# Kernel tuning notes

Measured on AMD Instinct MI355X. Metric: run time of the kernel, lower is better.

## Reference

```python
import jax, jax.numpy as jnp
import numpy as np


def setup_inputs() -> dict:
    key = jax.random.key(0)
    ks = jax.random.split(key, 7)
    B, T, H, O = 2048, 2048, 32, 2
    SCALE = 0.1  # keep gates out of deep saturation
    return {
        "x": jax.random.normal(ks[0], (B, T), dtype=jnp.float32),
        "w_ih": jax.random.normal(ks[1], (3 * H, 1), dtype=jnp.float32) * SCALE,
        "w_hh": jax.random.normal(ks[2], (3 * H, H), dtype=jnp.float32) * SCALE,
        "b_ih": jax.random.normal(ks[3], (3 * H,), dtype=jnp.float32) * SCALE,
        "b_hh": jax.random.normal(ks[4], (3 * H,), dtype=jnp.float32) * SCALE,
        "head_w": jax.random.normal(ks[5], (O, H), dtype=jnp.float32) * SCALE,
        "head_b": jax.random.normal(ks[6], (O,), dtype=jnp.float32) * SCALE,
    }


def reference(x, w_ih, w_hh, b_ih, b_hh, head_w, head_b):
    # x: [B, T] scalar time series (torch does x.unsqueeze(-1)).
    B, T = x.shape
    H = w_hh.shape[1]
    # Precompute input contributions to all 3 gates: [B, T, 3H]
    # (input_size == 1, so this is an outer product with w_ih[:, 0]).
    xg = x[:, :, None] * w_ih[:, 0] + b_ih
    xg_t = jnp.swapaxes(xg, 0, 1)  # [T, B, 3H] for scan

    def step(h, xg_step):
        gh = h @ w_hh.T + b_hh  # [B, 3H]
        xr, xz, xn = jnp.split(xg_step, 3, axis=-1)
        hr, hz, hn = jnp.split(gh, 3, axis=-1)
        r = jax.nn.sigmoid(xr + hr)
        z = jax.nn.sigmoid(xz + hz)
        n = jnp.tanh(xn + r * hn)
        h_new = (1.0 - z) * n + z * h
        return h_new, None

    h0 = jnp.zeros((B, H), dtype=x.dtype)
    hT, _ = jax.lax.scan(step, h0, xg_t)
    # head applied to last timestep's output (== final hidden state)
    return hT @ head_w.T + head_b
```

## Files before the change

kernel.cpp:

```cpp
#include <hip/hip_runtime.h>


typedef _Float16 f16x2 __attribute__((ext_vector_type(2)));

__device__ __forceinline__ float fdot2(int a, int b, float c) {
    return __builtin_amdgcn_fdot2(__builtin_bit_cast(f16x2, a),
                                  __builtin_bit_cast(f16x2, b), c, false);
}

__device__ __forceinline__ int pack_pair(float a, float b) {
    f16x2 p;
    p.x = (_Float16)a;
    p.y = (_Float16)b;
    return __builtin_bit_cast(int, p);
}

template<int CTRL>
__device__ __forceinline__ int dppmov(int src) {
    return __builtin_amdgcn_update_dpp(0, src, CTRL, 0xF, 0xF, true);
}

__global__ __launch_bounds__(64, 1)
void gru_scan_kernel(const float* __restrict__ x,
                     const float* __restrict__ w_ih,
                     const float* __restrict__ w_hh,
                     const float* __restrict__ b_ih,
                     const float* __restrict__ b_hh,
                     const float* __restrict__ head_w,
                     const float* __restrict__ head_b,
                     float* __restrict__ out,
                     int T)
{
    const int l  = (int)threadIdx.x;
    const int gg = (l >> 4) & 1;
    const int m  = (l & 15) + ((l >> 5) << 4);
    const int b  = (int)blockIdx.x * 2 + gg;

    __shared__ float hf_s[2][32];
    __shared__ __align__(16) float x_s[2][2][32];

    bool lowfirst;
    {
        auto pr = __builtin_amdgcn_permlane32_swap((unsigned)l, (unsigned)l,
                                                   false, false);
        lowfirst = ((int)pr[0] == (l & 31));
    }

    const float NL2E  = -1.44269504088896f;
    const float P2L2E =  2.88539008177793f;

    constexpr int M[16] = {0,1,2,3,7,6,5,4,15,14,13,12,8,9,10,11};
    const int c0 = l & 15;

    int wR[16], wZ[16], wN[16];
    {
        const float* pR = w_hh + (     m) * 32;
        const float* pZ = w_hh + (32 + m) * 32;
        const float* pN = w_hh + (64 + m) * 32;
#pragma unroll
        for (int q = 0; q < 16; ++q) {
            const int cc  = c0 ^ M[q];
            const int clo = lowfirst ? cc      : cc + 16;
            const int chi = lowfirst ? cc + 16 : cc;
            wR[q] = pack_pair(NL2E  * pR[clo], NL2E  * pR[chi]);
            wZ[q] = pack_pair(NL2E  * pZ[clo], NL2E  * pZ[chi]);
            wN[q] = pack_pair(P2L2E * pN[clo], P2L2E * pN[chi]);
        }
    }
#pragma unroll
    for (int q = 0; q < 16; ++q) {
        asm volatile("" : "+v"(wR[q]), "+v"(wZ[q]), "+v"(wN[q]));
    }

    const float wihr = NL2E  * w_ih[m];
    const float wihz = NL2E  * w_ih[32 + m];
    const float wihn = P2L2E * w_ih[64 + m];
    const float br   = NL2E  * (b_ih[m]      + b_hh[m]);
    const float bz   = NL2E  * (b_ih[32 + m] + b_hh[32 + m]);
    const float bni  = P2L2E * b_ih[64 + m];
    const float bnh  = P2L2E * b_hh[64 + m];

    const float* xrow   = x + (size_t)b * (size_t)T;
    const int    nchunk = T >> 5;

    float h = 0.0f;
    x_s[gg][0][m] = xrow[m];
    float xnext  = (nchunk > 1) ? xrow[32 + m] : 0.0f;
    __builtin_amdgcn_wave_barrier();

    for (int c = 0; c < nchunk; ++c) {
        const int buf = c & 1;
        const float* xs = &x_s[gg][buf][0];
#pragma unroll 4
        for (int s = 0; s < 32; ++s) {
            const float xv  = xs[s];
            const float hm1 = h - 1.0f;

            const unsigned hf = (unsigned)__builtin_bit_cast(unsigned short,
                                                             (_Float16)h);
            auto sw = __builtin_amdgcn_permlane32_swap(hf, hf, false, false);
            const int o0 = (int)sw[0];
            const int o1 = (int)sw[1];
            const int P0  = (o1 << 16) | o0;
            const int P1  = dppmov<0xB1 >(P0);
            const int P2  = dppmov<0x4E >(P0);
            const int P3  = dppmov<0x4E >(P1);
            const int P4  = dppmov<0x141>(P0);
            const int P5  = dppmov<0x141>(P1);
            const int P6  = dppmov<0x141>(P2);
            const int P7  = dppmov<0x141>(P3);
            const int P8  = dppmov<0x140>(P0);
            const int P9  = dppmov<0x140>(P1);
            const int P10 = dppmov<0x140>(P2);
            const int P11 = dppmov<0x140>(P3);
            const int P12 = dppmov<0x140>(P4);
            const int P13 = dppmov<0x140>(P5);
            const int P14 = dppmov<0x140>(P6);
            const int P15 = dppmov<0x140>(P7);

            float rA = fdot2(P0, wR[0], fmaf(xv, wihr, br));
            float zA = fdot2(P0, wZ[0], fmaf(xv, wihz, bz));
            float nA = fdot2(P0, wN[0], bnh);
            float rB = fdot2(P8, wR[8], 0.0f);
            float zB = fdot2(P8, wZ[8], 0.0f);
            float nB = fdot2(P8, wN[8], 0.0f);
            rA = fdot2(P1, wR[1], rA); zA = fdot2(P1, wZ[1], zA); nA = fdot2(P1, wN[1], nA);
            rB = fdot2(P9, wR[9], rB); zB = fdot2(P9, wZ[9], zB); nB = fdot2(P9, wN[9], nB);
            rA = fdot2(P2, wR[2], rA); zA = fdot2(P2, wZ[2], zA); nA = fdot2(P2, wN[2], nA);
            rB = fdot2(P10, wR[10], rB); zB = fdot2(P10, wZ[10], zB); nB = fdot2(P10, wN[10], nB);
            rA = fdot2(P3, wR[3], rA); zA = fdot2(P3, wZ[3], zA); nA = fdot2(P3, wN[3], nA);
            rB = fdot2(P11, wR[11], rB); zB = fdot2(P11, wZ[11], zB); nB = fdot2(P11, wN[11], nB);
            rA = fdot2(P4, wR[4], rA); zA = fdot2(P4, wZ[4], zA); nA = fdot2(P4, wN[4], nA);
            rB = fdot2(P12, wR[12], rB); zB = fdot2(P12, wZ[12], zB); nB = fdot2(P12, wN[12], nB);
            rA = fdot2(P5, wR[5], rA); zA = fdot2(P5, wZ[5], zA); nA = fdot2(P5, wN[5], nA);
            rB = fdot2(P13, wR[13], rB); zB = fdot2(P13, wZ[13], zB); nB = fdot2(P13, wN[13], nB);
            rA = fdot2(P6, wR[6], rA); zA = fdot2(P6, wZ[6], zA); nA = fdot2(P6, wN[6], nA);
            rB = fdot2(P14, wR[14], rB); zB = fdot2(P14, wZ[14], zB); nB = fdot2(P14, wN[14], nB);
            rA = fdot2(P7, wR[7], rA); zA = fdot2(P7, wZ[7], zA); nA = fdot2(P7, wN[7], nA);
            rB = fdot2(P15, wR[15], rB); zB = fdot2(P15, wZ[15], zB); nB = fdot2(P15, wN[15], nB);

            const float rp = rA + rB;
            const float zp = zA + zB;
            const float np = nA + nB;
            const float er = __builtin_amdgcn_exp2f(rp);
            const float ez = __builtin_amdgcn_exp2f(zp);
            const float r  = __builtin_amdgcn_rcpf(1.0f + er);
            const float z  = __builtin_amdgcn_rcpf(1.0f + ez);
            const float m2omz = fmaf(2.0f, z, -2.0f);
            const float ohz   = fmaf(z, hm1, 1.0f);
            const float u  = fmaf(r, np, fmaf(xv, wihn, bni));
            const float et = __builtin_amdgcn_exp2f(u);
            const float ti = __builtin_amdgcn_rcpf(1.0f + et);
            h = fmaf(m2omz, ti, ohz);
        }
        if (c + 1 < nchunk) {
            x_s[gg][1 - buf][m] = xnext;
            if (c + 2 < nchunk) xnext = xrow[(c + 2) * 32 + m];
            __builtin_amdgcn_wave_barrier();
        }
    }

    hf_s[gg][m] = h;
    __builtin_amdgcn_wave_barrier();
    if (l < 4) {
        const int g2 = l >> 1, o = l & 1;
        float acc = head_b[o];
        const float* hw = head_w + o * 32;
#pragma unroll
        for (int k = 0; k < 32; ++k) acc = fmaf(hf_s[g2][k], hw[k], acc);
        out[((int)blockIdx.x * 2 + g2) * 2 + o] = acc;
    }
}

extern "C" void kernel_launch(void* const* d_in, const int* in_sizes, int n_in,
                              void* d_out, int out_size, void* d_ws, size_t ws_size,
                              hipStream_t stream) {
    const float* x      = (const float*)d_in[0];
    const float* w_ih   = (const float*)d_in[1];
    const float* w_hh   = (const float*)d_in[2];
    const float* b_ih   = (const float*)d_in[3];
    const float* b_hh   = (const float*)d_in[4];
    const float* head_w = (const float*)d_in[5];
    const float* head_b = (const float*)d_in[6];
    float* out = (float*)d_out;

    const int B = out_size / 2;
    const int T = in_sizes[0] / B;

    dim3 grid(B / 2), block(64);
    hipLaunchKernelGGL(gru_scan_kernel, grid, block, 0, stream,
                       x, w_ih, w_hh, b_ih, b_hh, head_w, head_b, out, T);
}
```

Measured before the change: 449.6 us.

## Broadcast x from registers via readlane and split dot chains three ways

Replaces the per-step LDS reads of the input series with register-resident 64-element chunks for both batch rows, broadcast each step through readlane plus a per-lane select. This removes LDS traffic and wave barriers from the serial recurrence. The fdot2 accumulation is also regrouped from two chains of eight into three shorter chains (6/5/5) to cut the critical-path latency. The cost is an extra readlane, a select and one more add per gate each step.

```diff
diff --git a/kernel.cpp b/kernel.cpp
--- a/kernel.cpp
+++ b/kernel.cpp
@@ -34,10 +34,8 @@
     const int l  = (int)threadIdx.x;
     const int gg = (l >> 4) & 1;
     const int m  = (l & 15) + ((l >> 5) << 4);
-    const int b  = (int)blockIdx.x * 2 + gg;
 
     __shared__ float hf_s[2][32];
-    __shared__ __align__(16) float x_s[2][2][32];
 
     bool lowfirst;
     {
@@ -80,20 +78,26 @@
     const float bni  = P2L2E * b_ih[64 + m];
     const float bnh  = P2L2E * b_hh[64 + m];
 
-    const float* xrow   = x + (size_t)b * (size_t)T;
-    const int    nchunk = T >> 5;
+    const float* xrowA = x + (size_t)((int)blockIdx.x * 2    ) * (size_t)T;
+    const float* xrowB = x + (size_t)((int)blockIdx.x * 2 + 1) * (size_t)T;
+    const int    nchunk = T >> 6;
 
     float h = 0.0f;
-    x_s[gg][0][m] = xrow[m];
-    float xnext  = (nchunk > 1) ? xrow[32 + m] : 0.0f;
-    __builtin_amdgcn_wave_barrier();
+    float xcA = xrowA[l];
+    float xcB = xrowB[l];
+    float xnA = (nchunk > 1) ? xrowA[64 + l] : 0.0f;
+    float xnB = (nchunk > 1) ? xrowB[64 + l] : 0.0f;
 
     for (int c = 0; c < nchunk; ++c) {
-        const int buf = c & 1;
-        const float* xs = &x_s[gg][buf][0];
+        const int xbitsA = __builtin_bit_cast(int, xcA);
+        const int xbitsB = __builtin_bit_cast(int, xcB);
 #pragma unroll 4
-        for (int s = 0; s < 32; ++s) {
-            const float xv  = xs[s];
+        for (int s = 0; s < 64; ++s) {
+            const float xvA = __builtin_bit_cast(float,
+                                 __builtin_amdgcn_readlane(xbitsA, s));
+            const float xvB = __builtin_bit_cast(float,
+                                 __builtin_amdgcn_readlane(xbitsB, s));
+            const float xv  = gg ? xvB : xvA;
             const float hm1 = h - 1.0f;
 
             const unsigned hf = (unsigned)__builtin_bit_cast(unsigned short,
@@ -118,30 +122,63 @@
             const int P14 = dppmov<0x140>(P6);
             const int P15 = dppmov<0x140>(P7);
 
-            float rA = fdot2(P0, wR[0], fmaf(xv, wihr, br));
-            float zA = fdot2(P0, wZ[0], fmaf(xv, wihz, bz));
-            float nA = fdot2(P0, wN[0], bnh);
-            float rB = fdot2(P8, wR[8], 0.0f);
-            float zB = fdot2(P8, wZ[8], 0.0f);
-            float nB = fdot2(P8, wN[8], 0.0f);
-            rA = fdot2(P1, wR[1], rA); zA = fdot2(P1, wZ[1], zA); nA = fdot2(P1, wN[1], nA);
-            rB = fdot2(P9, wR[9], rB); zB = fdot2(P9, wZ[9], zB); nB = fdot2(P9, wN[9], nB);
-            rA = fdot2(P2, wR[2], rA); zA = fdot2(P2, wZ[2], zA); nA = fdot2(P2, wN[2], nA);
-            rB = fdot2(P10, wR[10], rB); zB = fdot2(P10, wZ[10], zB); nB = fdot2(P10, wN[10], nB);
-            rA = fdot2(P3, wR[3], rA); zA = fdot2(P3, wZ[3], zA); nA = fdot2(P3, wN[3], nA);
-            rB = fdot2(P11, wR[11], rB); zB = fdot2(P11, wZ[11], zB); nB = fdot2(P11, wN[11], nB);
-            rA = fdot2(P4, wR[4], rA); zA = fdot2(P4, wZ[4], zA); nA = fdot2(P4, wN[4], nA);
-            rB = fdot2(P12, wR[12], rB); zB = fdot2(P12, wZ[12], zB); nB = fdot2(P12, wN[12], nB);
-            rA = fdot2(P5, wR[5], rA); zA = fdot2(P5, wZ[5], zA); nA = fdot2(P5, wN[5], nA);
-            rB = fdot2(P13, wR[13], rB); zB = fdot2(P13, wZ[13], zB); nB = fdot2(P13, wN[13], nB);
-            rA = fdot2(P6, wR[6], rA); zA = fdot2(P6, wZ[6], zA); nA = fdot2(P6, wN[6], nA);
-            rB = fdot2(P14, wR[14], rB); zB = fdot2(P14, wZ[14], zB); nB = fdot2(P14, wN[14], nB);
-            rA = fdot2(P7, wR[7], rA); zA = fdot2(P7, wZ[7], zA); nA = fdot2(P7, wN[7], nA);
-            rB = fdot2(P15, wR[15], rB); zB = fdot2(P15, wZ[15], zB); nB = fdot2(P15, wN[15], nB);
-
-            const float rp = rA + rB;
-            const float zp = zA + zB;
-            const float np = nA + nB;
+            float rA = fdot2(P0,  wR[ 0], fmaf(xv, wihr, br));
+            float zA = fdot2(P0,  wZ[ 0], fmaf(xv, wihz, bz));
+            float nA = fdot2(P0,  wN[ 0], bnh);
+            float rB = fdot2(P6,  wR[ 6], 0.0f);
+            float zB = fdot2(P6,  wZ[ 6], 0.0f);
+            float nB = fdot2(P6,  wN[ 6], 0.0f);
+            float rC = fdot2(P11, wR[11], 0.0f);
+            float zC = fdot2(P11, wZ[11], 0.0f);
+            float nC = fdot2(P11, wN[11], 0.0f);
+
+            rA = fdot2(P1,  wR[ 1], rA);
+            zA = fdot2(P1,  wZ[ 1], zA);
+            nA = fdot2(P1,  wN[ 1], nA);
+            rB = fdot2(P7,  wR[ 7], rB);
+            zB = fdot2(P7,  wZ[ 7], zB);
+            nB = fdot2(P7,  wN[ 7], nB);
+            rC = fdot2(P12, wR[12], rC);
+            zC = fdot2(P12, wZ[12], zC);
+            nC = fdot2(P12, wN[12], nC);
+
+            rA = fdot2(P2,  wR[ 2], rA);
+            zA = fdot2(P2,  wZ[ 2], zA);
+            nA = fdot2(P2,  wN[ 2], nA);
+            rB = fdot2(P8,  wR[ 8], rB);
+            zB = fdot2(P8,  wZ[ 8], zB);
+            nB = fdot2(P8,  wN[ 8], nB);
+            rC = fdot2(P13, wR[13], rC);
+            zC = fdot2(P13, wZ[13], zC);
+            nC = fdot2(P13, wN[13], nC);
+
+            rA = fdot2(P3,  wR[ 3], rA);
+            zA = fdot2(P3,  wZ[ 3], zA);
+            nA = fdot2(P3,  wN[ 3], nA);
+            rB = fdot2(P9,  wR[ 9], rB);
+            zB = fdot2(P9,  wZ[ 9], zB);
+            nB = fdot2(P9,  wN[ 9], nB);
+            rC = fdot2(P14, wR[14], rC);
+            zC = fdot2(P14, wZ[14], zC);
+            nC = fdot2(P14, wN[14], nC);
+
+            rA = fdot2(P4,  wR[ 4], rA);
+            zA = fdot2(P4,  wZ[ 4], zA);
+            nA = fdot2(P4,  wN[ 4], nA);
+            rB = fdot2(P10, wR[10], rB);
+            zB = fdot2(P10, wZ[10], zB);
+            nB = fdot2(P10, wN[10], nB);
+            rC = fdot2(P15, wR[15], rC);
+            zC = fdot2(P15, wZ[15], zC);
+            nC = fdot2(P15, wN[15], nC);
+
+            rA = fdot2(P5,  wR[ 5], rA);
+            zA = fdot2(P5,  wZ[ 5], zA);
+            nA = fdot2(P5,  wN[ 5], nA);
+
+            const float rp = (rA + rB) + rC;
+            const float zp = (zA + zB) + zC;
+            const float np = (nA + nB) + nC;
             const float er = __builtin_amdgcn_exp2f(rp);
             const float ez = __builtin_amdgcn_exp2f(zp);
             const float r  = __builtin_amdgcn_rcpf(1.0f + er);
@@ -153,15 +190,17 @@
             const float ti = __builtin_amdgcn_rcpf(1.0f + et);
             h = fmaf(m2omz, ti, ohz);
         }
-        if (c + 1 < nchunk) {
-            x_s[gg][1 - buf][m] = xnext;
-            if (c + 2 < nchunk) xnext = xrow[(c + 2) * 32 + m];
-            __builtin_amdgcn_wave_barrier();
+        xcA = xnA;
+        xcB = xnB;
+        if (c + 2 < nchunk) {
+            xnA = xrowA[(c + 2) * 64 + l];
+            xnB = xrowB[(c + 2) * 64 + l];
         }
     }
 
     hf_s[gg][m] = h;
     __builtin_amdgcn_wave_barrier();
+    __builtin_amdgcn_s_barrier();
     if (l < 4) {
         const int g2 = l >> 1, o = l & 1;
         float acc = head_b[o];
```

New measurement: 495.3 us. +10.1%, slower.

## Interleave two independent GRU recurrences per wave to hide latency

Applied to the files above, without the earlier changes.

Each 64-lane wave now processes four batch rows as two independent recurrence streams, interleaving their all-gather, dot-product and gate computations. Interleaving lets the dependent latency of the DPP shuffles and transcendental ops in one stream overlap with work from the other. The grid is halved accordingly, and the unroll factor is reduced to limit register pressure. The risks are fewer waves available for hardware-level latency hiding and possible register spills.

```diff
diff --git a/kernel.cpp b/kernel.cpp
--- a/kernel.cpp
+++ b/kernel.cpp
@@ -19,6 +19,94 @@
 __device__ __forceinline__ int dppmov(int src) {
     return __builtin_amdgcn_update_dpp(0, src, CTRL, 0xF, 0xF, true);
 }
+
+#define ALLGATHER(S)                                                          \
+    const unsigned hf##S = (unsigned)__builtin_bit_cast(unsigned short,       \
+                                                        (_Float16)h##S);      \
+    auto sw##S = __builtin_amdgcn_permlane32_swap(hf##S, hf##S, false, false);\
+    const int P0_##S  = ((int)sw##S[1] << 16) | (int)sw##S[0];                \
+    const int P1_##S  = dppmov<0xB1 >(P0_##S);                                \
+    const int P2_##S  = dppmov<0x4E >(P0_##S);                                \
+    const int P3_##S  = dppmov<0x4E >(P1_##S);                                \
+    const int P4_##S  = dppmov<0x141>(P0_##S);                                \
+    const int P5_##S  = dppmov<0x141>(P1_##S);                                \
+    const int P6_##S  = dppmov<0x141>(P2_##S);                                \
+    const int P7_##S  = dppmov<0x141>(P3_##S);                                \
+    const int P8_##S  = dppmov<0x140>(P0_##S);                                \
+    const int P9_##S  = dppmov<0x140>(P1_##S);                                \
+    const int P10_##S = dppmov<0x140>(P2_##S);                                \
+    const int P11_##S = dppmov<0x140>(P3_##S);                                \
+    const int P12_##S = dppmov<0x140>(P4_##S);                                \
+    const int P13_##S = dppmov<0x140>(P5_##S);                                \
+    const int P14_##S = dppmov<0x140>(P6_##S);                                \
+    const int P15_##S = dppmov<0x140>(P7_##S);
+
+#define DOTS(S, XV)                                                           \
+    float rA##S = fdot2(P0_##S,  wR[ 0], fmaf((XV), wihr, br));               \
+    float zA##S = fdot2(P0_##S,  wZ[ 0], fmaf((XV), wihz, bz));               \
+    float nA##S = fdot2(P0_##S,  wN[ 0], bnh);                                \
+    float rB##S = fdot2(P8_##S,  wR[ 8], 0.0f);                               \
+    float zB##S = fdot2(P8_##S,  wZ[ 8], 0.0f);                               \
+    float nB##S = fdot2(P8_##S,  wN[ 8], 0.0f);                               \
+    rA##S = fdot2(P1_##S,  wR[ 1], rA##S);                                    \
+    zA##S = fdot2(P1_##S,  wZ[ 1], zA##S);                                    \
+    nA##S = fdot2(P1_##S,  wN[ 1], nA##S);                                    \
+    rB##S = fdot2(P9_##S,  wR[ 9], rB##S);                                    \
+    zB##S = fdot2(P9_##S,  wZ[ 9], zB##S);                                    \
+    nB##S = fdot2(P9_##S,  wN[ 9], nB##S);                                    \
+    rA##S = fdot2(P2_##S,  wR[ 2], rA##S);                                    \
+    zA##S = fdot2(P2_##S,  wZ[ 2], zA##S);                                    \
+    nA##S = fdot2(P2_##S,  wN[ 2], nA##S);                                    \
+    rB##S = fdot2(P10_##S, wR[10], rB##S);                                    \
+    zB##S = fdot2(P10_##S, wZ[10], zB##S);                                    \
+    nB##S = fdot2(P10_##S, wN[10], nB##S);                                    \
+    rA##S = fdot2(P3_##S,  wR[ 3], rA##S);                                    \
+    zA##S = fdot2(P3_##S,  wZ[ 3], zA##S);                                    \
+    nA##S = fdot2(P3_##S,  wN[ 3], nA##S);                                    \
+    rB##S = fdot2(P11_##S, wR[11], rB##S);                                    \
+    zB##S = fdot2(P11_##S, wZ[11], zB##S);                                    \
+    nB##S = fdot2(P11_##S, wN[11], nB##S);                                    \
+    rA##S = fdot2(P4_##S,  wR[ 4], rA##S);                                    \
+    zA##S = fdot2(P4_##S,  wZ[ 4], zA##S);                                    \
+    nA##S = fdot2(P4_##S,  wN[ 4], nA##S);                                    \
+    rB##S = fdot2(P12_##S, wR[12], rB##S);                                    \
+    zB##S = fdot2(P12_##S, wZ[12], zB##S);                                    \
+    nB##S = fdot2(P12_##S, wN[12], nB##S);                                    \
+    rA##S = fdot2(P5_##S,  wR[ 5], rA##S);                                    \
+    zA##S = fdot2(P5_##S,  wZ[ 5], zA##S);                                    \
+    nA##S = fdot2(P5_##S,  wN[ 5], nA##S);                                    \
+    rB##S = fdot2(P13_##S, wR[13], rB##S);                                    \
+    zB##S = fdot2(P13_##S, wZ[13], zB##S);                                    \
+    nB##S = fdot2(P13_##S, wN[13], nB##S);                                    \
+    rA##S = fdot2(P6_##S,  wR[ 6], rA##S);                                    \
+    zA##S = fdot2(P6_##S,  wZ[ 6], zA##S);                                    \
+    nA##S = fdot2(P6_##S,  wN[ 6], nA##S);                                    \
+    rB##S = fdot2(P14_##S, wR[14], rB##S);                                    \
+    zB##S = fdot2(P14_##S, wZ[14], zB##S);                                    \
+    nB##S = fdot2(P14_##S, wN[14], nB##S);                                    \
+    rA##S = fdot2(P7_##S,  wR[ 7], rA##S);                                    \
+    zA##S = fdot2(P7_##S,  wZ[ 7], zA##S);                                    \
+    nA##S = fdot2(P7_##S,  wN[ 7], nA##S);                                    \
+    rB##S = fdot2(P15_##S, wR[15], rB##S);                                    \
+    zB##S = fdot2(P15_##S, wZ[15], zB##S);                                    \
+    nB##S = fdot2(P15_##S, wN[15], nB##S);
+
+#define TAIL(S, XV)                                                           \
+    {                                                                         \
+        const float rp = rA##S + rB##S;                                       \
+        const float zp = zA##S + zB##S;                                       \
+        const float np = nA##S + nB##S;                                       \
+        const float er = __builtin_amdgcn_exp2f(rp);                          \
+        const float ez = __builtin_amdgcn_exp2f(zp);                          \
+        const float r  = __builtin_amdgcn_rcpf(1.0f + er);                    \
+        const float z  = __builtin_amdgcn_rcpf(1.0f + ez);                    \
+        const float m2omz = fmaf(2.0f, z, -2.0f);                             \
+        const float ohz   = fmaf(z, hm1##S, 1.0f);                            \
+        const float u  = fmaf(r, np, fmaf((XV), wihn, bni));                  \
+        const float et = __builtin_amdgcn_exp2f(u);                           \
+        const float ti = __builtin_amdgcn_rcpf(1.0f + et);                    \
+        h##S = fmaf(m2omz, ti, ohz);                                          \
+    }
 
 __global__ __launch_bounds__(64, 1)
 void gru_scan_kernel(const float* __restrict__ x,
@@ -34,10 +122,9 @@
     const int l  = (int)threadIdx.x;
     const int gg = (l >> 4) & 1;
     const int m  = (l & 15) + ((l >> 5) << 4);
-    const int b  = (int)blockIdx.x * 2 + gg;
-
-    __shared__ float hf_s[2][32];
-    __shared__ __align__(16) float x_s[2][2][32];
+
+    __shared__ float hf_s[4][32];
+    __shared__ __align__(16) float x_s[4][2][32];
 
     bool lowfirst;
     {
@@ -80,95 +167,56 @@
     const float bni  = P2L2E * b_ih[64 + m];
     const float bnh  = P2L2E * b_hh[64 + m];
 
-    const float* xrow   = x + (size_t)b * (size_t)T;
+    const float* xrow0 = x + (size_t)((int)blockIdx.x * 4 + gg    ) * (size_t)T;
+    const float* xrow1 = x + (size_t)((int)blockIdx.x * 4 + 2 + gg) * (size_t)T;
     const int    nchunk = T >> 5;
 
-    float h = 0.0f;
-    x_s[gg][0][m] = xrow[m];
-    float xnext  = (nchunk > 1) ? xrow[32 + m] : 0.0f;
+    float h0 = 0.0f, h1 = 0.0f;
+    x_s[gg    ][0][m] = xrow0[m];
+    x_s[2 + gg][0][m] = xrow1[m];
+    float xnext0 = (nchunk > 1) ? xrow0[32 + m] : 0.0f;
+    float xnext1 = (nchunk > 1) ? xrow1[32 + m] : 0.0f;
     __builtin_amdgcn_wave_barrier();
 
     for (int c = 0; c < nchunk; ++c) {
         const int buf = c & 1;
-        const float* xs = &x_s[gg][buf][0];
-#pragma unroll 4
+        const float* xs0 = &x_s[gg    ][buf][0];
+        const float* xs1 = &x_s[2 + gg][buf][0];
+#pragma unroll 2
         for (int s = 0; s < 32; ++s) {
-            const float xv  = xs[s];
-            const float hm1 = h - 1.0f;
-
-            const unsigned hf = (unsigned)__builtin_bit_cast(unsigned short,
-                                                             (_Float16)h);
-            auto sw = __builtin_amdgcn_permlane32_swap(hf, hf, false, false);
-            const int o0 = (int)sw[0];
-            const int o1 = (int)sw[1];
-            const int P0  = (o1 << 16) | o0;
-            const int P1  = dppmov<0xB1 >(P0);
-            const int P2  = dppmov<0x4E >(P0);
-            const int P3  = dppmov<0x4E >(P1);
-            const int P4  = dppmov<0x141>(P0);
-            const int P5  = dppmov<0x141>(P1);
-            const int P6  = dppmov<0x141>(P2);
-            const int P7  = dppmov<0x141>(P3);
-            const int P8  = dppmov<0x140>(P0);
-            const int P9  = dppmov<0x140>(P1);
-            const int P10 = dppmov<0x140>(P2);
-            const int P11 = dppmov<0x140>(P3);
-            const int P12 = dppmov<0x140>(P4);
-            const int P13 = dppmov<0x140>(P5);
-            const int P14 = dppmov<0x140>(P6);
-            const int P15 = dppmov<0x140>(P7);
-
-            float rA = fdot2(P0, wR[0], fmaf(xv, wihr, br));
-            float zA = fdot2(P0, wZ[0], fmaf(xv, wihz, bz));
-            float nA = fdot2(P0, wN[0], bnh);
-            float rB = fdot2(P8, wR[8], 0.0f);
-            float zB = fdot2(P8, wZ[8], 0.0f);
-            float nB = fdot2(P8, wN[8], 0.0f);
-            rA = fdot2(P1, wR[1], rA); zA = fdot2(P1, wZ[1], zA); nA = fdot2(P1, wN[1], nA);
-            rB = fdot2(P9, wR[9], rB); zB = fdot2(P9, wZ[9], zB); nB = fdot2(P9, wN[9], nB);
-            rA = fdot2(P2, wR[2], rA); zA = fdot2(P2, wZ[2], zA); nA = fdot2(P2, wN[2], nA);
-            rB = fdot2(P10, wR[10], rB); zB = fdot2(P10, wZ[10], zB); nB = fdot2(P10, wN[10], nB);
-            rA = fdot2(P3, wR[3], rA); zA = fdot2(P3, wZ[3], zA); nA = fdot2(P3, wN[3], nA);
-            rB = fdot2(P11, wR[11], rB); zB = fdot2(P11, wZ[11], zB); nB = fdot2(P11, wN[11], nB);
-            rA = fdot2(P4, wR[4], rA); zA = fdot2(P4, wZ[4], zA); nA = fdot2(P4, wN[4], nA);
-            rB = fdot2(P12, wR[12], rB); zB = fdot2(P12, wZ[12], zB); nB = fdot2(P12, wN[12], nB);
-            rA = fdot2(P5, wR[5], rA); zA = fdot2(P5, wZ[5], zA); nA = fdot2(P5, wN[5], nA);
-            rB = fdot2(P13, wR[13], rB); zB = fdot2(P13, wZ[13], zB); nB = fdot2(P13, wN[13], nB);
-            rA = fdot2(P6, wR[6], rA); zA = fdot2(P6, wZ[6], zA); nA = fdot2(P6, wN[6], nA);
-            rB = fdot2(P14, wR[14], rB); zB = fdot2(P14, wZ[14], zB); nB = fdot2(P14, wN[14], nB);
-            rA = fdot2(P7, wR[7], rA); zA = fdot2(P7, wZ[7], zA); nA = fdot2(P7, wN[7], nA);
-            rB = fdot2(P15, wR[15], rB); zB = fdot2(P15, wZ[15], zB); nB = fdot2(P15, wN[15], nB);
-
-            const float rp = rA + rB;
-            const float zp = zA + zB;
-            const float np = nA + nB;
-            const float er = __builtin_amdgcn_exp2f(rp);
-            const float ez = __builtin_amdgcn_exp2f(zp);
-            const float r  = __builtin_amdgcn_rcpf(1.0f + er);
-            const float z  = __builtin_amdgcn_rcpf(1.0f + ez);
-            const float m2omz = fmaf(2.0f, z, -2.0f);
-            const float ohz   = fmaf(z, hm1, 1.0f);
-            const float u  = fmaf(r, np, fmaf(xv, wihn, bni));
-            const float et = __builtin_amdgcn_exp2f(u);
-            const float ti = __builtin_amdgcn_rcpf(1.0f + et);
-            h = fmaf(m2omz, ti, ohz);
+            const float xv0  = xs0[s];
+            const float xv1  = xs1[s];
+            const float hm10 = h0 - 1.0f;
+            const float hm11 = h1 - 1.0f;
+
+            ALLGATHER(0)
+            DOTS(0, xv0)
+            ALLGATHER(1)
+            DOTS(1, xv1)
+            TAIL(0, xv0)
+            TAIL(1, xv1)
         }
         if (c + 1 < nchunk) {
-            x_s[gg][1 - buf][m] = xnext;
-            if (c + 2 < nchunk) xnext = xrow[(c + 2) * 32 + m];
+            x_s[gg    ][1 - buf][m] = xnext0;
+            x_s[2 + gg][1 - buf][m] = xnext1;
+            if (c + 2 < nchunk) {
+                xnext0 = xrow0[(c + 2) * 32 + m];
+                xnext1 = xrow1[(c + 2) * 32 + m];
+            }
             __builtin_amdgcn_wave_barrier();
         }
     }
 
-    hf_s[gg][m] = h;
+    hf_s[gg    ][m] = h0;
+    hf_s[2 + gg][m] = h1;
     __builtin_amdgcn_wave_barrier();
-    if (l < 4) {
+    if (l < 8) {
         const int g2 = l >> 1, o = l & 1;
         float acc = head_b[o];
         const float* hw = head_w + o * 32;
 #pragma unroll
         for (int k = 0; k < 32; ++k) acc = fmaf(hf_s[g2][k], hw[k], acc);
-        out[((int)blockIdx.x * 2 + g2) * 2 + o] = acc;
+        out[((int)blockIdx.x * 4 + g2) * 2 + o] = acc;
     }
 }
 
@@ -187,7 +235,7 @@
     const int B = out_size / 2;
     const int T = in_sizes[0] / B;
 
-    dim3 grid(B / 2), block(64);
+    dim3 grid(B / 4), block(64);
     hipLaunchKernelGGL(gru_scan_kernel, grid, block, 0, stream,
                        x, w_ih, w_hh, b_ih, b_hh, head_w, head_b, out, T);
 }
```

After: 786.5 us. 74.9% more time.
